# Optimization experiments

Measured on AMD Instinct MI355X. Metric: run time of the kernel, lower is better.

Reference implementation:

```python
import jax, jax.numpy as jnp
import numpy as np
from jax import lax

DIM, HEADS, HID = 192, 8, int(192 * 2.66)  # HID = 510
B, H, W = 8, 128, 128


def _ln(x, w, b):
    # WithBias LayerNorm over channel dim (to_3d puts C last, so per-pixel over C)
    mu = x.mean(1, keepdims=True)
    var = ((x - mu) ** 2).mean(1, keepdims=True)
    return (x - mu) / jnp.sqrt(var + 1e-5) * w[None, :, None, None] + b[None, :, None, None]


def _c1(x, w):  # 1x1 conv, w: [O, C]
    return jnp.einsum('bchw,oc->bohw', x, w)


def _dw(x, w):  # depthwise 3x3, w: [C, 1, 3, 3]
    return lax.conv_general_dilated(x, w, (1, 1), 'SAME',
                                    dimension_numbers=('NCHW', 'OIHW', 'NCHW'),
                                    feature_group_count=x.shape[1])


def _film(x, k_v, Wk):
    m = k_v @ Wk.T                       # [b, 2c]
    c = x.shape[1]
    return x * m[:, :c, None, None] + m[:, c:, None, None]


def _double_norm(t):
    # custom_normalize (norm + eps) followed by F.normalize (max(norm, eps)), dim=-1
    n1 = jnp.sqrt((t * t).sum(-1, keepdims=True)) + 1e-12
    t = t / n1
    n2 = jnp.sqrt((t * t).sum(-1, keepdims=True))
    return t / jnp.maximum(n2, 1e-12)


def setup_inputs() -> dict:
    key = jax.random.key(0)
    ks = jax.random.split(key, 12)
    s = 0.05
    return {
        'x': jax.random.normal(ks[0], (B, DIM, H, W), jnp.float32),
        'k_v': jax.random.normal(ks[1], (B, 256), jnp.float32),
        'ln1_w': jnp.ones((DIM,), jnp.float32),
        'ln1_b': jnp.zeros((DIM,), jnp.float32),
        'attn_kern': jax.random.normal(ks[2], (2 * DIM, 256), jnp.float32) * 0.02,
        'qkv_w': jax.random.normal(ks[3], (3 * DIM, DIM), jnp.float32) * s,
        'qkv_dw_w': jax.random.normal(ks[4], (3 * DIM, 1, 3, 3), jnp.float32) * s,
        'proj_w': jax.random.normal(ks[5], (DIM, DIM), jnp.float32) * s,
        'temperature': jnp.ones((HEADS, 1, 1), jnp.float32),
        'ln2_w': jnp.ones((DIM,), jnp.float32),
        'ln2_b': jnp.zeros((DIM,), jnp.float32),
        'ffn_kern': jax.random.normal(ks[6], (2 * DIM, 256), jnp.float32) * 0.02,
        'pin_w': jax.random.normal(ks[7], (2 * HID, DIM), jnp.float32) * s,
        'ffn_dw_w': jax.random.normal(ks[8], (2 * HID, 1, 3, 3), jnp.float32) * s,
        'pout_w': jax.random.normal(ks[9], (DIM, HID), jnp.float32) * s,
    }


def reference(x, k_v, ln1_w, ln1_b, attn_kern, qkv_w, qkv_dw_w, proj_w, temperature,
              ln2_w, ln2_b, ffn_kern, pin_w, ffn_dw_w, pout_w):
    b, c, h, w = x.shape
    cf = c // HEADS

    # ---- attention branch ----
    xn = _film(_ln(x, ln1_w, ln1_b), k_v, attn_kern)
    qkv = _dw(_c1(xn, qkv_w), qkv_dw_w)              # [b, 3c, h, w]
    q, k, v = jnp.split(qkv, 3, axis=1)
    q = _double_norm(q.reshape(b, HEADS, cf, h * w))
    k = _double_norm(k.reshape(b, HEADS, cf, h * w))
    v = v.reshape(b, HEADS, cf, h * w)
    attn = jnp.einsum('bhcn,bhdn->bhcd', q, k) * temperature  # channel attention [b,H,cf,cf]
    attn = jax.nn.softmax(attn, axis=-1)
    out = jnp.einsum('bhcd,bhdn->bhcn', attn, v).reshape(b, c, h, w)
    x = x + _c1(out, proj_w)

    # ---- gated conv FFN branch ----
    xn = _film(_ln(x, ln2_w, ln2_b), k_v, ffn_kern)
    u = _dw(_c1(xn, pin_w), ffn_dw_w)                # [b, 2*HID, h, w]
    u1, u2 = jnp.split(u, 2, axis=1)
    u = jax.nn.gelu(u1, approximate=False) * u2
    x = x + _c1(u, pout_w)
    return x  # k_v passes through unchanged
```

## Files before the change

kernel.cpp:

```cpp
#include <hip/hip_runtime.h>
#include <math.h>

#define NB 8
#define NC 192
#define NHEADS 8
#define NCF 24
#define NHW 16384
#define NWID 128
#define CQKV 576
#define OQKV_PAD 640
#define CPIN 1024
#define CG 512
#define OM_PAD 256

typedef unsigned short bfu;
typedef _Float16 f16x8 __attribute__((ext_vector_type(8)));
typedef _Float16 f16x2 __attribute__((ext_vector_type(2)));
typedef float f32x4 __attribute__((ext_vector_type(4)));

__device__ __forceinline__ unsigned short f2h(float f) {
    _Float16 h = (_Float16)f;
    return __builtin_bit_cast(unsigned short, h);
}
__device__ __forceinline__ float h2f(unsigned short u) {
    return (float)__builtin_bit_cast(_Float16, u);
}
__device__ __forceinline__ float gelu_tanh(float x) {
    float x3 = x * x * x;
    float z = 0.7978845608028654f * fmaf(0.044715f, x3, x);
    float e = __expf(2.f * z);
    float th = 1.f - 2.f / (e + 1.f);
    return 0.5f * x * (1.f + th);
}

struct F8 { float v[8]; };
union H8 { uint4 u; f16x2 h[4]; };
__device__ __forceinline__ F8 loadh8(const bfu* p) {
    uint4 r = *(const uint4*)p;
    F8 o;
    o.v[0] = h2f((unsigned short)(r.x & 0xffff)); o.v[1] = h2f((unsigned short)(r.x >> 16));
    o.v[2] = h2f((unsigned short)(r.y & 0xffff)); o.v[3] = h2f((unsigned short)(r.y >> 16));
    o.v[4] = h2f((unsigned short)(r.z & 0xffff)); o.v[5] = h2f((unsigned short)(r.z >> 16));
    o.v[6] = h2f((unsigned short)(r.w & 0xffff)); o.v[7] = h2f((unsigned short)(r.w >> 16));
    return o;
}
__device__ __forceinline__ void storeh8(bfu* p, const float* a) {
    uint4 r;
    r.x = (unsigned)f2h(a[0]) | ((unsigned)f2h(a[1]) << 16);
    r.y = (unsigned)f2h(a[2]) | ((unsigned)f2h(a[3]) << 16);
    r.z = (unsigned)f2h(a[4]) | ((unsigned)f2h(a[5]) << 16);
    r.w = (unsigned)f2h(a[6]) | ((unsigned)f2h(a[7]) << 16);
    *(uint4*)p = r;
}
__device__ __forceinline__ f16x2 h2z() {
    f16x2 z; z[0] = (_Float16)0.f; z[1] = (_Float16)0.f; return z;
}

__global__ __launch_bounds__(256) void zfill(float* __restrict__ p, int n) {
    int i = blockIdx.x * 256 + threadIdx.x;
    if (i < n) p[i] = 0.f;
}

__global__ __launch_bounds__(256) void prep_film(
    const float* __restrict__ kv, const float* __restrict__ kern,
    const float* __restrict__ lnw, const float* __restrict__ lnb,
    float* __restrict__ sArr, float* __restrict__ tArr)
{
    const int b = blockIdx.y;
    const int wave = threadIdx.x >> 6, lane = threadIdx.x & 63;
    const int r = blockIdx.x * 4 + wave;
    const float* kvb = kv + b * 256;
    float4 kvv = *(const float4*)(kvb + lane * 4);
    float4 k1 = *(const float4*)(kern + (size_t)r * 256 + lane * 4);
    float4 k2 = *(const float4*)(kern + (size_t)(r + NC) * 256 + lane * 4);
    float d1 = kvv.x * k1.x + kvv.y * k1.y + kvv.z * k1.z + kvv.w * k1.w;
    float d2 = kvv.x * k2.x + kvv.y * k2.y + kvv.z * k2.z + kvv.w * k2.w;
    #pragma unroll
    for (int off = 32; off; off >>= 1) {
        d1 += __shfl_down(d1, off, 64);
        d2 += __shfl_down(d2, off, 64);
    }
    if (lane == 0) {
        sArr[b * NC + r] = lnw[r] * d1;
        tArr[b * NC + r] = lnb[r] * d1 + d2;
    }
}

__global__ __launch_bounds__(256) void wprep(
    const float* __restrict__ W, const float* __restrict__ sA, const float* __restrict__ tA,
    bfu* __restrict__ Abf, float* __restrict__ u, float* __restrict__ v0, int mode)
{
    const int wave = threadIdx.x >> 6, lane = threadIdx.x & 63;
    const int o = blockIdx.x * 4 + wave;
    const int b = blockIdx.y;
    const int Opad = (mode == 0) ? OQKV_PAD : (mode == 1 ? CPIN : OM_PAD);
    const int K = (mode == 2) ? 512 : 192;
    const int Kr = (mode == 2) ? 510 : 192;
    const int K32 = K >> 5;
    int src;
    if (mode == 0) src = (o < 576) ? o : -1;
    else if (mode == 1) src = (o < 510) ? o : (o < 512 ? -1 : (o < 1022 ? o - 2 : -1));
    else src = (o < 192) ? o : -1;
    const float* wr = (src >= 0) ? W + (size_t)src * Kr : nullptr;
    const float* sb = sA + b * NC;
    const float* tb = tA + b * NC;
    bfu* abase = Abf + (size_t)b * Opad * K;
    float au = 0.f, av = 0.f;
    for (int c0 = lane * 4; c0 < K; c0 += 256) {
        float a[4] = {0.f, 0.f, 0.f, 0.f};
        if (src >= 0) {
            #pragma unroll
            for (int j = 0; j < 4; ++j) {
                int c = c0 + j;
                if (c < Kr) {
                    float w = wr[c];
                    if (mode == 2) a[j] = w;
                    else { a[j] = w * sb[c]; av = fmaf(w, tb[c], av); }
                }
            }
        }
        ushort4 pk;
        bfu b0 = f2h(a[0]), b1 = f2h(a[1]), b2 = f2h(a[2]), b3 = f2h(a[3]);
        pk.x = b0; pk.y = b1; pk.z = b2; pk.w = b3;
        au += h2f(b0) + h2f(b1) + h2f(b2) + h2f(b3);
        int frag = (o >> 4) * K32 + (c0 >> 5);
        int within = ((c0 >> 3) & 3) * 128 + (o & 15) * 8 + (c0 & 7);
        *(ushort4*)(abase + (size_t)frag * 512 + within) = pk;
    }
    if (mode < 2) {
        #pragma unroll
        for (int off = 32; off; off >>= 1) {
            au += __shfl_down(au, off, 64);
            av += __shfl_down(av, off, 64);
        }
        if (lane == 0) {
            u[(size_t)b * Opad + o] = au;
            v0[(size_t)b * Opad + o] = (src >= 0) ? av : 0.f;
        }
    }
}

__global__ __launch_bounds__(256) void wdw_prep(
    const float* __restrict__ src, bfu* __restrict__ dstT, int C, int mode)
{
    int i = blockIdx.x * 256 + threadIdx.x;
    if (i >= 9 * C) return;
    int tap = i / C, col = i % C;
    float v;
    if (mode == 0) v = src[(size_t)col * 9 + tap];
    else {
        if (col < 512) v = (col < 510) ? src[(size_t)col * 9 + tap] : 0.f;
        else { int c2 = col - 512; v = (c2 < 510) ? src[(size_t)(510 + c2) * 9 + tap] : 0.f; }
    }
    dstT[(size_t)tap * C + col] = f2h(v);
}

__global__ __launch_bounds__(256) void ln_cvt_cm(
    const float* __restrict__ x, float* __restrict__ mu, float* __restrict__ rstd,
    bfu* __restrict__ xbf, int cb)
{
    __shared__ bfu lt[64][198];
    const int blkpx = blockIdx.x;
    const int b = blkpx >> 8;
    const int n0 = (blkpx & 255) * 64;
    const int tid = threadIdx.x;
    #pragma unroll
    for (int it = 0; it < 12; ++it) {
        int task = it * 256 + tid;
        int c = task >> 4, q = task & 15;
        float4 v = *(const float4*)(x + ((size_t)b * NC + c) * NHW + n0 + q * 4);
        lt[q * 4 + 0][c] = f2h(v.x);
        lt[q * 4 + 1][c] = f2h(v.y);
        lt[q * 4 + 2][c] = f2h(v.z);
        lt[q * 4 + 3][c] = f2h(v.w);
    }
    __syncthreads();
    {
        int px = tid >> 2, part = tid & 3;
        const unsigned* row = (const unsigned*)&lt[px][0];
        float s = 0.f, ss = 0.f;
        #pragma unroll
        for (int i = 0; i < 24; ++i) {
            unsigned w = row[part * 24 + i];
            float a = h2f((unsigned short)(w & 0xffff));
            float bb = h2f((unsigned short)(w >> 16));
            s += a + bb; ss = fmaf(a, a, ss); ss = fmaf(bb, bb, ss);
        }
        s += __shfl_down(s, 2, 4); ss += __shfl_down(ss, 2, 4);
        s += __shfl_down(s, 1, 4); ss += __shfl_down(ss, 1, 4);
        if (part == 0) {
            int idx = b * NHW + n0 + px;
            float m = s * (1.f / 192.f);
            float var = ss * (1.f / 192.f) - m * m;
            mu[idx] = m;
            rstd[idx] = rsqrtf(var + 1e-5f);
        }
    }
    #pragma unroll
    for (int it = 0; it < 6; ++it) {
        int task = it * 256 + tid;
        int px = task / 24, ckk = task % 24;
        const unsigned* row = (const unsigned*)&lt[px][0];
        uint4 o;
        o.x = row[ckk * 4 + 0]; o.y = row[ckk * 4 + 1];
        o.z = row[ckk * 4 + 2]; o.w = row[ckk * 4 + 3];
        *(uint4*)(xbf + ((size_t)b * NHW + n0 + px) * NC + ckk * 8) = o;
    }
}

__global__ __launch_bounds__(256) void ln_stats_pm8(
    const bfu* __restrict__ xpm, float* __restrict__ mu, float* __restrict__ rstd, int cb)
{
    int gt = blockIdx.x * 256 + threadIdx.x;
    int px = gt >> 3, seg = gt & 7;
    if (px >= cb * NHW) return;
    const bfu* row = xpm + (size_t)px * NC;
    float s = 0.f, ss = 0.f;
    #pragma unroll
    for (int it = 0; it < 3; ++it) {
        F8 v = loadh8(row + (seg + it * 8) * 8);
        #pragma unroll
        for (int j = 0; j < 8; ++j) { s += v.v[j]; ss = fmaf(v.v[j], v.v[j], ss); }
    }
    #pragma unroll
    for (int off = 4; off; off >>= 1) {
        s += __shfl_down(s, off, 8);
        ss += __shfl_down(ss, off, 8);
    }
    if (seg == 0) {
        float m = s * (1.f / 192.f);
        float var = ss * (1.f / 192.f) - m * m;
        mu[px] = m;
        rstd[px] = rsqrtf(var + 1e-5f);
    }
}

template<int EPI>
__global__ __launch_bounds__(256) void gemm_pm(
    const bfu* __restrict__ A, long aBStride, int Opad, int Oreal, int K,
    const bfu* __restrict__ X, int xRow, int xOff,
    void* __restrict__ Y, int yRow,
    const void* __restrict__ res, int resRow,
    const float* __restrict__ mu, const float* __restrict__ rstd,
    const float* __restrict__ uvec, const float* __restrict__ v0vec, int uStride)
{
    constexpr bool FULLK = (EPI != 3);
    constexpr int SMEMSZ = FULLK ? (64 * 208 * 2) : 33024;
    __shared__ __align__(16) char smem[SMEMSZ];
    bfu* xs = (bfu*)smem;
    bfu (*stg)[136] = (bfu(*)[136])smem;
    float (*stg32)[129] = (float(*)[129])smem;

    const int b = blockIdx.z;
    const int om = blockIdx.y * 128;
    const int n0 = blockIdx.x * 64;
    const int tid = threadIdx.x;
    const int lane = tid & 63, wave = tid >> 6;
    const int wy = wave >> 1, wx = wave & 1;
    const int l15 = lane & 15, kg = lane >> 4;
    const int K32 = K >> 5;
    const int o16b = (om >> 4) + wy * 4;

    const bfu* Ab = A + (size_t)b * aBStride;
    const bfu* Xbase = X + ((size_t)b * NHW + n0) * xRow + xOff;

    f32x4 acc[4][2];
    #pragma unroll
    for (int i = 0; i < 4; ++i)
        #pragma unroll
        for (int j = 0; j < 2; ++j) acc[i][j] = (f32x4){0.f, 0.f, 0.f, 0.f};

    if constexpr (FULLK) {
        #pragma unroll
        for (int i = 0; i < 6; ++i) {
            int task = i * 256 + tid;
            int r = task / 24, c = task % 24;
            uint4 v = *(const uint4*)(Xbase + (size_t)r * xRow + c * 8);
            *(uint4*)&xs[r * 208 + c * 8] = v;
        }
        __syncthreads();
        #pragma unroll
        for (int k32 = 0; k32 < 6; ++k32) {
            f16x8 af[4], bfr[2];
            #pragma unroll
            for (int mf = 0; mf < 4; ++mf)
                af[mf] = *(const f16x8*)(Ab + ((size_t)(o16b + mf) * 6 + k32) * 512 + lane * 8);
            #pragma unroll
            for (int nf = 0; nf < 2; ++nf)
                bfr[nf] = *(const f16x8*)&xs[(wx * 32 + nf * 16 + l15) * 208 + k32 * 32 + kg * 8];
            #pragma unroll
            for (int mf = 0; mf < 4; ++mf)
                #pragma unroll
                for (int nf = 0; nf < 2; ++nf)
                    acc[mf][nf] = __builtin_amdgcn_mfma_f32_16x16x32_f16(af[mf], bfr[nf], acc[mf][nf], 0, 0, 0);
        }
        __syncthreads();
    } else {
        const int sr = tid >> 3, sc = tid & 7;
        const int NCH = K >> 6;
        #pragma unroll
        for (int i = 0; i < 2; ++i) {
            int r = i * 32 + sr;
            uint4 v = *(const uint4*)(Xbase + (size_t)r * xRow + sc * 8);
            *(uint4*)&xs[r * 72 + sc * 8] = v;
        }
        __syncthreads();
        for (int kc = 0; kc < NCH; ++kc) {
            const int cur = kc & 1;
            if (kc + 1 < NCH) {
                #pragma unroll
                for (int i = 0; i < 2; ++i) {
                    int r = i * 32 + sr;
                    uint4 v = *(const uint4*)(Xbase + (size_t)r * xRow + (kc + 1) * 64 + sc * 8);
                    *(uint4*)&xs[((cur ^ 1) * 64 + r) * 72 + sc * 8] = v;
                }
            }
            #pragma unroll
            for (int ks = 0; ks < 2; ++ks) {
                const int k32 = kc * 2 + ks;
                f16x8 af[4], bfr[2];
                #pragma unroll
                for (int mf = 0; mf < 4; ++mf)
                    af[mf] = *(const f16x8*)(Ab + ((size_t)(o16b + mf) * K32 + k32) * 512 + lane * 8);
                #pragma unroll
                for (int nf = 0; nf < 2; ++nf)
                    bfr[nf] = *(const f16x8*)&xs[(cur * 64 + wx * 32 + nf * 16 + l15) * 72 + ks * 32 + kg * 8];
                #pragma unroll
                for (int mf = 0; mf < 4; ++mf)
                    #pragma unroll
                    for (int nf = 0; nf < 2; ++nf)
                        acc[mf][nf] = __builtin_amdgcn_mfma_f32_16x16x32_f16(af[mf], bfr[nf], acc[mf][nf], 0, 0, 0);
            }
            __syncthreads();
        }
    }

    #pragma unroll
    for (int nf = 0; nf < 2; ++nf) {
        const int nl = wx * 32 + nf * 16 + l15;
        float muv = 0.f, rsv = 0.f;
        if (EPI == 0) {
            muv = mu[(size_t)b * NHW + n0 + nl];
            rsv = rstd[(size_t)b * NHW + n0 + nl];
        }
        #pragma unroll
        for (int mf = 0; mf < 4; ++mf) {
            const int obl = wy * 64 + mf * 16 + kg * 4;
            if (EPI == 3) {
                stg32[nl][obl + 0] = acc[mf][nf][0];
                stg32[nl][obl + 1] = acc[mf][nf][1];
                stg32[nl][obl + 2] = acc[mf][nf][2];
                stg32[nl][obl + 3] = acc[mf][nf][3];
            } else {
                float r0, r1, r2, r3;
                if (EPI == 0) {
                    float4 uv = *(const float4*)(uvec + (size_t)b * uStride + om + obl);
                    float4 vv = *(const float4*)(v0vec + (size_t)b * uStride + om + obl);
                    r0 = rsv * (acc[mf][nf][0] - muv * uv.x) + vv.x;
                    r1 = rsv * (acc[mf][nf][1] - muv * uv.y) + vv.y;
                    r2 = rsv * (acc[mf][nf][2] - muv * uv.z) + vv.z;
                    r3 = rsv * (acc[mf][nf][3] - muv * uv.w) + vv.w;
                } else {
                    r0 = acc[mf][nf][0]; r1 = acc[mf][nf][1];
                    r2 = acc[mf][nf][2]; r3 = acc[mf][nf][3];
                }
                ushort4 pk;
                pk.x = f2h(r0); pk.y = f2h(r1); pk.z = f2h(r2); pk.w = f2h(r3);
                *(ushort4*)&stg[nl][obl] = pk;
            }
        }
    }
    __syncthreads();

    if (EPI == 3) {
        #pragma unroll
        for (int it = 0; it < 8; ++it) {
            int task = it * 256 + tid;
            int o = task >> 4, q = task & 15;
            int oc = om + o;
            if (oc >= Oreal) continue;
            float vals[4];
            #pragma unroll
            for (int j = 0; j < 4; ++j) {
                float v = stg32[q * 4 + j][o];
                float r = h2f(((const bfu*)res)[((size_t)b * NHW + n0 + q * 4 + j) * resRow + oc]);
                vals[j] = v + r;
            }
            *(float4*)((float*)Y + ((size_t)b * NC + oc) * NHW + n0 + q * 4) =
                make_float4(vals[0], vals[1], vals[2], vals[3]);
        }
    } else {
        #pragma unroll
        for (int it = 0; it < 4; ++it) {
            int task = it * 256 + tid;
            int nl = task >> 4, ch = task & 15;
            int oc = om + ch * 8;
            if (oc >= Oreal) continue;
            uint4 sv = *(const uint4*)&stg[nl][ch * 8];
            size_t nglob = (size_t)b * NHW + n0 + nl;
            if (EPI == 0) {
                *(uint4*)((bfu*)Y + nglob * yRow + oc) = sv;
            } else {
                float a[8];
                a[0] = h2f((unsigned short)(sv.x & 0xffff)); a[1] = h2f((unsigned short)(sv.x >> 16));
                a[2] = h2f((unsigned short)(sv.y & 0xffff)); a[3] = h2f((unsigned short)(sv.y >> 16));
                a[4] = h2f((unsigned short)(sv.z & 0xffff)); a[5] = h2f((unsigned short)(sv.z >> 16));
                a[6] = h2f((unsigned short)(sv.w & 0xffff)); a[7] = h2f((unsigned short)(sv.w >> 16));
                F8 rv = loadh8((const bfu*)res + nglob * resRow + oc);
                #pragma unroll
                for (int j = 0; j < 8; ++j) a[j] += rv.v[j];
                storeh8((bfu*)Y + nglob * yRow + oc, a);
            }
        }
    }
}

template<int CIN>
__global__ __launch_bounds__(256) void dw_pm8(
    const bfu* __restrict__ in, const bfu* __restrict__ wT, bfu* __restrict__ out, int cb)
{
    const int CHUNKS = CIN / 8;
    const int NPB = NHW / 8;
    int f = blockIdx.x * 256 + threadIdx.x;
    if (f >= cb * NPB * CHUNKS) return;
    int ch = f % CHUNKS;
    int pb = f / CHUNKS;
    int n8 = pb & (NPB - 1);
    int b  = pb >> 11;
    int xq = n8 & 15, y = n8 >> 4;
    int x0 = xq * 8;
    const int c8 = ch * 8;
    const bfu* rowb = in + ((size_t)b * NHW + (size_t)y * NWID) * CIN + c8;

    f16x2 acc[8][4];
    #pragma unroll
    for (int j = 0; j < 8; ++j)
        #pragma unroll
        for (int q = 0; q < 4; ++q) acc[j][q] = h2z();

    #pragma unroll
    for (int dy = -1; dy <= 1; ++dy) {
        int yy = y + dy;
        if ((unsigned)yy >= (unsigned)NWID) continue;
        const bfu* rb = rowb + (long)dy * NWID * CIN;
        f16x2 w1[3][4];
        #pragma unroll
        for (int t = 0; t < 3; ++t) {
            H8 wv; wv.u = *(const uint4*)(wT + (size_t)((dy + 1) * 3 + t) * CIN + c8);
            #pragma unroll
            for (int q = 0; q < 4; ++q) w1[t][q] = wv.h[q];
        }
        #pragma unroll
        for (int c = 0; c < 10; ++c) {
            int xx = x0 - 1 + c;
            if ((unsigned)xx >= (unsigned)NWID) continue;
            H8 v; v.u = *(const uint4*)(rb + (size_t)xx * CIN);
            #pragma unroll
            for (int j = 0; j < 8; ++j) {
                int t = c - j;
                if (t < 0 || t > 2) continue;
                #pragma unroll
                for (int q = 0; q < 4; ++q)
                    acc[j][q] = w1[t][q] * v.h[q] + acc[j][q];
            }
        }
    }
    #pragma unroll
    for (int j = 0; j < 8; ++j) {
        H8 o;
        #pragma unroll
        for (int q = 0; q < 4; ++q) o.h[q] = acc[j][q];
        *(uint4*)(out + ((size_t)b * NHW + (size_t)y * NWID + x0 + j) * CIN + c8) = o.u;
    }
}

template<int CIN, int COUT>
__global__ __launch_bounds__(256) void dw_gate(
    const bfu* __restrict__ in, const bfu* __restrict__ wT, bfu* __restrict__ out, int cb)
{
    const int CHUNKS = COUT / 8;
    const int NPB = NHW / 4;
    int f = blockIdx.x * 256 + threadIdx.x;
    if (f >= cb * NPB * CHUNKS) return;
    int ch = f % CHUNKS;
    int pb = f / CHUNKS;
    int n4 = pb & (NPB - 1);
    int b  = pb >> 12;
    int xb = n4 & 31, y = n4 >> 5;
    int x0 = xb * 4;
    const int c8 = ch * 8;
    const bfu* rowb = in + ((size_t)b * NHW + (size_t)y * NWID) * CIN + c8;

    f16x2 a1[4][4], a2[4][4];
    #pragma unroll
    for (int j = 0; j < 4; ++j)
        #pragma unroll
        for (int q = 0; q < 4; ++q) { a1[j][q] = h2z(); a2[j][q] = h2z(); }

    #pragma unroll
    for (int dy = -1; dy <= 1; ++dy) {
        int yy = y + dy;
        if ((unsigned)yy >= (unsigned)NWID) continue;
        const bfu* rb = rowb + (long)dy * NWID * CIN;
        f16x2 w1[3][4], w2[3][4];
        #pragma unroll
        for (int t = 0; t < 3; ++t) {
            const bfu* wp = wT + (size_t)((dy + 1) * 3 + t) * CIN + c8;
            H8 wa; wa.u = *(const uint4*)wp;
            H8 wb; wb.u = *(const uint4*)(wp + 512);
            #pragma unroll
            for (int q = 0; q < 4; ++q) { w1[t][q] = wa.h[q]; w2[t][q] = wb.h[q]; }
        }
        #pragma unroll
        for (int c = 0; c < 6; ++c) {
            int xx = x0 - 1 + c;
            if ((unsigned)xx >= (unsigned)NWID) continue;
            H8 v1; v1.u = *(const uint4*)(rb + (size_t)xx * CIN);
            H8 v2; v2.u = *(const uint4*)(rb + (size_t)xx * CIN + 512);
            #pragma unroll
            for (int j = 0; j < 4; ++j) {
                int t = c - j;
                if (t < 0 || t > 2) continue;
                #pragma unroll
                for (int q = 0; q < 4; ++q) {
                    a1[j][q] = w1[t][q] * v1.h[q] + a1[j][q];
                    a2[j][q] = w2[t][q] * v2.h[q] + a2[j][q];
                }
            }
        }
    }
    #pragma unroll
    for (int j = 0; j < 4; ++j) {
        H8 o;
        #pragma unroll
        for (int q = 0; q < 4; ++q) {
            float g0 = gelu_tanh((float)a1[j][q][0]) * (float)a2[j][q][0];
            float g1 = gelu_tanh((float)a1[j][q][1]) * (float)a2[j][q][1];
            f16x2 r; r[0] = (_Float16)g0; r[1] = (_Float16)g1;
            o.h[q] = r;
        }
        *(uint4*)(out + ((size_t)b * NHW + (size_t)y * NWID + x0 + j) * COUT + c8) = o.u;
    }
}

__global__ __launch_bounds__(256) void gram_pm(
    const bfu* __restrict__ qkv, float* __restrict__ S32,
    float* __restrict__ Q2, float* __restrict__ K2, int b0)
{
    __shared__ bfu lds[392 * 72];
    const int b = blockIdx.y;
    const int nc = blockIdx.x;
    const int tid = threadIdx.x;
    const int lane = tid & 63, wave = tid >> 6;
    const int l15 = lane & 15, kg = lane >> 4;

    f32x4 sAcc[2][2][2], qAcc[2][2], kAcc[2][2];
    #pragma unroll
    for (int h = 0; h < 2; ++h)
        #pragma unroll
        for (int i = 0; i < 2; ++i) {
            qAcc[h][i] = (f32x4){0.f, 0.f, 0.f, 0.f};
            kAcc[h][i] = (f32x4){0.f, 0.f, 0.f, 0.f};
            #pragma unroll
            for (int j = 0; j < 2; ++j) sAcc[h][i][j] = (f32x4){0.f, 0.f, 0.f, 0.f};
        }

    const size_t pbase = (size_t)b * NHW + (size_t)nc * 256;
    unsigned* ldsw = (unsigned*)lds;

    for (int it = 0; it < 4; ++it) {
        const size_t nb = pbase + it * 64;
        #pragma unroll
        for (int i = 0; i < 6; ++i) {
            int task = i * 256 + tid;
            int np = task & 31, ch = task >> 5;
            const bfu* r0 = qkv + (nb + np * 2) * CQKV + ch * 8;
            uint4 v0 = *(const uint4*)r0;
            uint4 v1 = *(const uint4*)(r0 + CQKV);
            int cb8 = ch * 8;
            ldsw[(cb8 + 0) * 36 + np] = (v0.x & 0xffffu) | (v1.x << 16);
            ldsw[(cb8 + 1) * 36 + np] = (v0.x >> 16) | (v1.x & 0xffff0000u);
            ldsw[(cb8 + 2) * 36 + np] = (v0.y & 0xffffu) | (v1.y << 16);
            ldsw[(cb8 + 3) * 36 + np] = (v0.y >> 16) | (v1.y & 0xffff0000u);
            ldsw[(cb8 + 4) * 36 + np] = (v0.z & 0xffffu) | (v1.z << 16);
            ldsw[(cb8 + 5) * 36 + np] = (v0.z >> 16) | (v1.z & 0xffff0000u);
            ldsw[(cb8 + 6) * 36 + np] = (v0.w & 0xffffu) | (v1.w << 16);
            ldsw[(cb8 + 7) * 36 + np] = (v0.w >> 16) | (v1.w & 0xffff0000u);
        }
        ldsw[(384 + (tid >> 5)) * 36 + (tid & 31)] = 0;
        __syncthreads();
        #pragma unroll
        for (int hh = 0; hh < 2; ++hh) {
            const int h = wave * 2 + hh;
            const int qr = h * NCF, kr = NC + h * NCF;
            #pragma unroll
            for (int ks = 0; ks < 2; ++ks) {
                const int nsub = ks * 32 + kg * 8;
                f16x8 aq0 = *(const f16x8*)(lds + (qr + l15) * 72 + nsub);
                f16x8 aq1 = *(const f16x8*)(lds + (qr + 16 + l15) * 72 + nsub);
                f16x8 bk0 = *(const f16x8*)(lds + (kr + l15) * 72 + nsub);
                f16x8 bk1 = *(const f16x8*)(lds + (kr + 16 + l15) * 72 + nsub);
                sAcc[hh][0][0] = __builtin_amdgcn_mfma_f32_16x16x32_f16(aq0, bk0, sAcc[hh][0][0], 0, 0, 0);
                sAcc[hh][0][1] = __builtin_amdgcn_mfma_f32_16x16x32_f16(aq0, bk1, sAcc[hh][0][1], 0, 0, 0);
                sAcc[hh][1][0] = __builtin_amdgcn_mfma_f32_16x16x32_f16(aq1, bk0, sAcc[hh][1][0], 0, 0, 0);
                sAcc[hh][1][1] = __builtin_amdgcn_mfma_f32_16x16x32_f16(aq1, bk1, sAcc[hh][1][1], 0, 0, 0);
                qAcc[hh][0] = __builtin_amdgcn_mfma_f32_16x16x32_f16(aq0, aq0, qAcc[hh][0], 0, 0, 0);
                qAcc[hh][1] = __builtin_amdgcn_mfma_f32_16x16x32_f16(aq1, aq1, qAcc[hh][1], 0, 0, 0);
                kAcc[hh][0] = __builtin_amdgcn_mfma_f32_16x16x32_f16(bk0, bk0, kAcc[hh][0], 0, 0, 0);
                kAcc[hh][1] = __builtin_amdgcn_mfma_f32_16x16x32_f16(bk1, bk1, kAcc[hh][1], 0, 0, 0);
            }
        }
        __syncthreads();
    }

    const int gb = b0 + b;
    #pragma unroll
    for (int hh = 0; hh < 2; ++hh) {
        const int h = wave * 2 + hh;
        float* Sp = S32 + ((size_t)gb * NHEADS + h) * 1024;
        #pragma unroll
        for (int mt = 0; mt < 2; ++mt)
            #pragma unroll
            for (int nt = 0; nt < 2; ++nt)
                #pragma unroll
                for (int r = 0; r < 4; ++r) {
                    int c = mt * 16 + kg * 4 + r, d = nt * 16 + l15;
                    atomicAdd(&Sp[c * 32 + d], sAcc[hh][mt][nt][r]);
                }
        #pragma unroll
        for (int t = 0; t < 2; ++t)
            #pragma unroll
            for (int r = 0; r < 4; ++r) {
                int row = t * 16 + kg * 4 + r, col = t * 16 + l15;
                if (row == col && row < NCF) {
                    atomicAdd(&Q2[((size_t)gb * NHEADS + h) * NCF + row], qAcc[hh][t][r]);
                    atomicAdd(&K2[((size_t)gb * NHEADS + h) * NCF + row], kAcc[hh][t][r]);
                }
            }
    }
}

__global__ __launch_bounds__(256) void attn_fold(
    const float* __restrict__ S32, const float* __restrict__ Q2, const float* __restrict__ K2,
    const float* __restrict__ temp, const float* __restrict__ projw, bfu* __restrict__ Mbf, int b0)
{
    const int gb = b0 + blockIdx.x, tid = threadIdx.x;
    __shared__ float P[NHEADS * NCF * NCF];
    for (int e = tid; e < NHEADS * NCF * NCF; e += 256) {
        int h = e / (NCF * NCF);
        int r = e % (NCF * NCF);
        int c = r / NCF, d = r % NCF;
        float sv = S32[((size_t)gb * NHEADS + h) * 1024 + c * 32 + d];
        float rq = sqrtf(Q2[((size_t)gb * NHEADS + h) * NCF + c]);
        float rk = sqrtf(K2[((size_t)gb * NHEADS + h) * NCF + d]);
        P[e] = sv / (rq * rk) * temp[h];
    }
    __syncthreads();
    if (tid < NHEADS * NCF) {
        int h = tid / NCF, c = tid % NCF;
        float* row = P + h * (NCF * NCF) + c * NCF;
        float mx = row[0];
        #pragma unroll
        for (int d = 1; d < NCF; ++d) mx = fmaxf(mx, row[d]);
        float sum = 0.f;
        #pragma unroll
        for (int d = 0; d < NCF; ++d) { float e2 = __expf(row[d] - mx); row[d] = e2; sum += e2; }
        float inv = 1.f / sum;
        #pragma unroll
        for (int d = 0; d < NCF; ++d) row[d] *= inv;
    }
    __syncthreads();
    bfu* Mb = Mbf + (size_t)gb * OM_PAD * NC;
    if (tid < NC) {
        int o = tid;
        int o16 = o >> 4, l15o = o & 15;
        for (int h = 0; h < NHEADS; ++h) {
            float pw[NCF];
            #pragma unroll
            for (int c = 0; c < NCF; ++c) pw[c] = projw[(size_t)o * NC + h * NCF + c];
            #pragma unroll
            for (int d = 0; d < NCF; ++d) {
                float acc = 0.f;
                #pragma unroll
                for (int c = 0; c < NCF; ++c) acc = fmaf(pw[c], P[h * (NCF * NCF) + c * NCF + d], acc);
                int cc = h * NCF + d;
                int idx = (o16 * 6 + (cc >> 5)) * 512 + ((cc >> 3) & 3) * 128 + l15o * 8 + (cc & 7);
                Mb[idx] = f2h(acc);
            }
        }
    }
    for (int e = tid; e < (OM_PAD - NC) * NC; e += 256) Mb[NC * NC + e] = 0;
}

extern "C" void kernel_launch(void* const* d_in, const int* in_sizes, int n_in,
                              void* d_out, int out_size, void* d_ws, size_t ws_size,
                              hipStream_t stream)
{
    const float* x     = (const float*)d_in[0];
    const float* kv    = (const float*)d_in[1];
    const float* ln1w  = (const float*)d_in[2];
    const float* ln1b  = (const float*)d_in[3];
    const float* akern = (const float*)d_in[4];
    const float* qkvw  = (const float*)d_in[5];
    const float* qkvdw = (const float*)d_in[6];
    const float* projw = (const float*)d_in[7];
    const float* temp  = (const float*)d_in[8];
    const float* ln2w  = (const float*)d_in[9];
    const float* ln2b  = (const float*)d_in[10];
    const float* fkern = (const float*)d_in[11];
    const float* pinw  = (const float*)d_in[12];
    const float* ffndw = (const float*)d_in[13];
    const float* poutw = (const float*)d_in[14];
    float* out = (float*)d_out;

    char* wp = (char*)d_ws;
    size_t off = 0;
    auto take = [&](size_t bytes) {
        char* r = wp + off;
        off = (off + bytes + 255) & ~(size_t)255;
        return r;
    };
    float* mu1   = (float*)take((size_t)NB * NHW * 4);
    float* rstd1 = (float*)take((size_t)NB * NHW * 4);
    float* mu2   = (float*)take((size_t)NB * NHW * 4);
    float* rstd2 = (float*)take((size_t)NB * NHW * 4);
    float* s1 = (float*)take(NB * NC * 4);  float* t1 = (float*)take(NB * NC * 4);
    float* s2 = (float*)take(NB * NC * 4);  float* t2 = (float*)take(NB * NC * 4);
    bfu* A1 = (bfu*)take((size_t)NB * OQKV_PAD * 192 * 2);
    bfu* A2 = (bfu*)take((size_t)NB * CPIN * 192 * 2);
    bfu* A3 = (bfu*)take((size_t)OM_PAD * 512 * 2);
    bfu* Mbf = (bfu*)take((size_t)NB * OM_PAD * NC * 2);
    float* u1  = (float*)take((size_t)NB * OQKV_PAD * 4);
    float* v01 = (float*)take((size_t)NB * OQKV_PAD * 4);
    float* u2  = (float*)take((size_t)NB * CPIN * 4);
    float* v02 = (float*)take((size_t)NB * CPIN * 4);
    bfu* wdwT1 = (bfu*)take(9 * CQKV * 2);
    bfu* wdwT2 = (bfu*)take(9 * CPIN * 2);
    float* S32 = (float*)take((size_t)NB * NHEADS * 1024 * 4);
    float* Q2  = (float*)take((size_t)NB * NHEADS * NCF * 4);
    float* K2  = (float*)take((size_t)NB * NHEADS * NCF * 4);
    const size_t bigoff = off;

    const size_t PB = (size_t)NHW * (384 + 384 + 2048 + 1152);
    size_t avail = (ws_size > bigoff) ? ws_size - bigoff : 0;
    int CB = 8;
    while (CB > 1 && (size_t)CB * PB > avail) CB >>= 1;

    dim3 blk(256);

    prep_film<<<dim3(48, NB), blk, 0, stream>>>(kv, akern, ln1w, ln1b, s1, t1);
    prep_film<<<dim3(48, NB), blk, 0, stream>>>(kv, fkern, ln2w, ln2b, s2, t2);
    wprep<<<dim3(OQKV_PAD / 4, NB), blk, 0, stream>>>(qkvw, s1, t1, A1, u1, v01, 0);
    wprep<<<dim3(CPIN / 4, NB), blk, 0, stream>>>(pinw, s2, t2, A2, u2, v02, 1);
    wprep<<<dim3(OM_PAD / 4, 1), blk, 0, stream>>>(poutw, s1, t1, A3, nullptr, nullptr, 2);
    wdw_prep<<<(9 * CQKV + 255) / 256, blk, 0, stream>>>(qkvdw, wdwT1, CQKV, 0);
    wdw_prep<<<(9 * CPIN + 255) / 256, blk, 0, stream>>>(ffndw, wdwT2, CPIN, 1);
    {
        int nz = NB * NHEADS * 1024 + 2 * NB * NHEADS * NCF + 256;
        zfill<<<(nz + 255) / 256, blk, 0, stream>>>(S32, nz);
    }

    for (int b0 = 0; b0 < NB; b0 += CB) {
        bfu* bfX  = (bfu*)(wp + bigoff);
        bfu* out1 = (bfu*)(wp + bigoff + (size_t)CB * NHW * 384);
        char* big1 = wp + bigoff + (size_t)CB * NHW * 768;
        char* big2 = big1 + (size_t)CB * NHW * 2048;
        bfu* qkv_pre = (bfu*)big1;
        bfu* qkvb    = (bfu*)big2;
        bfu* u_pre   = (bfu*)big1;
        bfu* gbuf    = (bfu*)big2;

        const float* xb = x + (size_t)b0 * NC * NHW;
        float* mu1b = mu1 + (size_t)b0 * NHW;   float* rs1b = rstd1 + (size_t)b0 * NHW;
        float* mu2b = mu2 + (size_t)b0 * NHW;   float* rs2b = rstd2 + (size_t)b0 * NHW;

        ln_cvt_cm<<<CB * 256, blk, 0, stream>>>(xb, mu1b, rs1b, bfX, CB);
        gemm_pm<0><<<dim3(256, OQKV_PAD / 128, CB), blk, 0, stream>>>(
            A1 + (size_t)b0 * OQKV_PAD * 192, (long)OQKV_PAD * 192, OQKV_PAD, CQKV, 192,
            bfX, NC, 0, qkv_pre, CQKV, nullptr, 0,
            mu1b, rs1b, u1 + (size_t)b0 * OQKV_PAD, v01 + (size_t)b0 * OQKV_PAD, OQKV_PAD);
        dw_pm8<CQKV><<<CB * 576, blk, 0, stream>>>(qkv_pre, wdwT1, qkvb, CB);
        gram_pm<<<dim3(64, CB), blk, 0, stream>>>(qkvb, S32, Q2, K2, b0);
        attn_fold<<<CB, blk, 0, stream>>>(S32, Q2, K2, temp, projw, Mbf, b0);
        gemm_pm<1><<<dim3(256, OM_PAD / 128, CB), blk, 0, stream>>>(
            Mbf + (size_t)b0 * OM_PAD * NC, (long)OM_PAD * NC, OM_PAD, NC, 192,
            qkvb, CQKV, 384, out1, NC, bfX, NC,
            nullptr, nullptr, nullptr, nullptr, 0);

        ln_stats_pm8<<<CB * 512, blk, 0, stream>>>(out1, mu2b, rs2b, CB);
        gemm_pm<0><<<dim3(256, CPIN / 128, CB), blk, 0, stream>>>(
            A2 + (size_t)b0 * CPIN * 192, (long)CPIN * 192, CPIN, CPIN, 192,
            out1, NC, 0, u_pre, CPIN, nullptr, 0,
            mu2b, rs2b, u2 + (size_t)b0 * CPIN, v02 + (size_t)b0 * CPIN, CPIN);
        dw_gate<CPIN, CG><<<CB * (NHW / 4) * (CG / 8) / 256, blk, 0, stream>>>(
            u_pre, wdwT2, gbuf, CB);
        gemm_pm<3><<<dim3(256, OM_PAD / 128, CB), blk, 0, stream>>>(
            A3, 0, OM_PAD, NC, 512,
            gbuf, CG, 0, out + (size_t)b0 * NC * NHW, 0, out1, NC,
            nullptr, nullptr, nullptr, nullptr, 0);
    }
}
```

Before: 800.9 us.

## Fuse LayerNorm stats into GEMM, widen GEMM N-tile, and widen dw_gate pixel strip

LayerNorm mean/rstd computation moves out of ln_cvt_cm and the separate ln_stats_pm8 kernel and into the full-K GEMM. The GEMM now computes the statistics from its shared-memory X tile. The full-K GEMM tile grows from 64 to 128 pixels per block, doubling accumulators per wave and halving the grid. The depthwise gate kernel now processes 8 pixels per thread instead of 4, so each loaded input column is reused across more outputs. These changes remove a kernel launch and the global mu/rstd round-trips, at the cost of higher register use and more shared memory per block, which may lower occupancy.

```diff
diff --git a/kernel.cpp b/kernel.cpp
--- a/kernel.cpp
+++ b/kernel.cpp
@@ -156,8 +156,7 @@
 }
 
 __global__ __launch_bounds__(256) void ln_cvt_cm(
-    const float* __restrict__ x, float* __restrict__ mu, float* __restrict__ rstd,
-    bfu* __restrict__ xbf, int cb)
+    const float* __restrict__ x, bfu* __restrict__ xbf, int cb)
 {
     __shared__ bfu lt[64][198];
     const int blkpx = blockIdx.x;
@@ -175,27 +174,6 @@
         lt[q * 4 + 3][c] = f2h(v.w);
     }
     __syncthreads();
-    {
-        int px = tid >> 2, part = tid & 3;
-        const unsigned* row = (const unsigned*)&lt[px][0];
-        float s = 0.f, ss = 0.f;
-        #pragma unroll
-        for (int i = 0; i < 24; ++i) {
-            unsigned w = row[part * 24 + i];
-            float a = h2f((unsigned short)(w & 0xffff));
-            float bb = h2f((unsigned short)(w >> 16));
-            s += a + bb; ss = fmaf(a, a, ss); ss = fmaf(bb, bb, ss);
-        }
-        s += __shfl_down(s, 2, 4); ss += __shfl_down(ss, 2, 4);
-        s += __shfl_down(s, 1, 4); ss += __shfl_down(ss, 1, 4);
-        if (part == 0) {
-            int idx = b * NHW + n0 + px;
-            float m = s * (1.f / 192.f);
-            float var = ss * (1.f / 192.f) - m * m;
-            mu[idx] = m;
-            rstd[idx] = rsqrtf(var + 1e-5f);
-        }
-    }
     #pragma unroll
     for (int it = 0; it < 6; ++it) {
         int task = it * 256 + tid;
@@ -208,150 +186,96 @@
     }
 }
 
-__global__ __launch_bounds__(256) void ln_stats_pm8(
-    const bfu* __restrict__ xpm, float* __restrict__ mu, float* __restrict__ rstd, int cb)
-{
-    int gt = blockIdx.x * 256 + threadIdx.x;
-    int px = gt >> 3, seg = gt & 7;
-    if (px >= cb * NHW) return;
-    const bfu* row = xpm + (size_t)px * NC;
-    float s = 0.f, ss = 0.f;
-    #pragma unroll
-    for (int it = 0; it < 3; ++it) {
-        F8 v = loadh8(row + (seg + it * 8) * 8);
-        #pragma unroll
-        for (int j = 0; j < 8; ++j) { s += v.v[j]; ss = fmaf(v.v[j], v.v[j], ss); }
-    }
-    #pragma unroll
-    for (int off = 4; off; off >>= 1) {
-        s += __shfl_down(s, off, 8);
-        ss += __shfl_down(ss, off, 8);
-    }
-    if (seg == 0) {
-        float m = s * (1.f / 192.f);
-        float var = ss * (1.f / 192.f) - m * m;
-        mu[px] = m;
-        rstd[px] = rsqrtf(var + 1e-5f);
-    }
-}
-
 template<int EPI>
 __global__ __launch_bounds__(256) void gemm_pm(
     const bfu* __restrict__ A, long aBStride, int Opad, int Oreal, int K,
     const bfu* __restrict__ X, int xRow, int xOff,
     void* __restrict__ Y, int yRow,
     const void* __restrict__ res, int resRow,
-    const float* __restrict__ mu, const float* __restrict__ rstd,
     const float* __restrict__ uvec, const float* __restrict__ v0vec, int uStride)
 {
     constexpr bool FULLK = (EPI != 3);
-    constexpr int SMEMSZ = FULLK ? (64 * 208 * 2) : 33024;
+    constexpr int SMEMSZ = FULLK ? (128 * 200 * 2 + 128 * 8) : 33024;
     __shared__ __align__(16) char smem[SMEMSZ];
     bfu* xs = (bfu*)smem;
     bfu (*stg)[136] = (bfu(*)[136])smem;
     float (*stg32)[129] = (float(*)[129])smem;
+    float* smu = (float*)(smem + 128 * 200 * 2);
+    float* srs = smu + 128;
 
     const int b = blockIdx.z;
     const int om = blockIdx.y * 128;
-    const int n0 = blockIdx.x * 64;
     const int tid = threadIdx.x;
     const int lane = tid & 63, wave = tid >> 6;
     const int wy = wave >> 1, wx = wave & 1;
     const int l15 = lane & 15, kg = lane >> 4;
     const int K32 = K >> 5;
     const int o16b = (om >> 4) + wy * 4;
-
     const bfu* Ab = A + (size_t)b * aBStride;
-    const bfu* Xbase = X + ((size_t)b * NHW + n0) * xRow + xOff;
-
-    f32x4 acc[4][2];
-    #pragma unroll
-    for (int i = 0; i < 4; ++i)
-        #pragma unroll
-        for (int j = 0; j < 2; ++j) acc[i][j] = (f32x4){0.f, 0.f, 0.f, 0.f};
 
     if constexpr (FULLK) {
-        #pragma unroll
-        for (int i = 0; i < 6; ++i) {
+        const int n0 = blockIdx.x * 128;
+        const bfu* Xbase = X + ((size_t)b * NHW + n0) * xRow + xOff;
+
+        f32x4 acc[4][4];
+        #pragma unroll
+        for (int i = 0; i < 4; ++i)
+            #pragma unroll
+            for (int j = 0; j < 4; ++j) acc[i][j] = (f32x4){0.f, 0.f, 0.f, 0.f};
+
+        #pragma unroll
+        for (int i = 0; i < 12; ++i) {
             int task = i * 256 + tid;
             int r = task / 24, c = task % 24;
             uint4 v = *(const uint4*)(Xbase + (size_t)r * xRow + c * 8);
-            *(uint4*)&xs[r * 208 + c * 8] = v;
+            *(uint4*)&xs[r * 200 + c * 8] = v;
         }
         __syncthreads();
+
+        if (EPI == 0) {
+            int px = tid >> 1, hh = tid & 1;
+            float s = 0.f, ss = 0.f;
+            #pragma unroll
+            for (int i = 0; i < 12; ++i) {
+                F8 v = loadh8(xs + px * 200 + hh * 96 + i * 8);
+                #pragma unroll
+                for (int j = 0; j < 8; ++j) { s += v.v[j]; ss = fmaf(v.v[j], v.v[j], ss); }
+            }
+            s += __shfl_xor(s, 1, 64);
+            ss += __shfl_xor(ss, 1, 64);
+            if (hh == 0) {
+                float m = s * (1.f / 192.f);
+                float var = ss * (1.f / 192.f) - m * m;
+                smu[px] = m;
+                srs[px] = rsqrtf(var + 1e-5f);
+            }
+        }
+
         #pragma unroll
         for (int k32 = 0; k32 < 6; ++k32) {
-            f16x8 af[4], bfr[2];
+            f16x8 af[4], bfr[4];
             #pragma unroll
             for (int mf = 0; mf < 4; ++mf)
                 af[mf] = *(const f16x8*)(Ab + ((size_t)(o16b + mf) * 6 + k32) * 512 + lane * 8);
             #pragma unroll
-            for (int nf = 0; nf < 2; ++nf)
-                bfr[nf] = *(const f16x8*)&xs[(wx * 32 + nf * 16 + l15) * 208 + k32 * 32 + kg * 8];
+            for (int nf = 0; nf < 4; ++nf)
+                bfr[nf] = *(const f16x8*)&xs[(wx * 64 + nf * 16 + l15) * 200 + k32 * 32 + kg * 8];
             #pragma unroll
             for (int mf = 0; mf < 4; ++mf)
                 #pragma unroll
-                for (int nf = 0; nf < 2; ++nf)
+                for (int nf = 0; nf < 4; ++nf)
                     acc[mf][nf] = __builtin_amdgcn_mfma_f32_16x16x32_f16(af[mf], bfr[nf], acc[mf][nf], 0, 0, 0);
         }
         __syncthreads();
-    } else {
-        const int sr = tid >> 3, sc = tid & 7;
-        const int NCH = K >> 6;
-        #pragma unroll
-        for (int i = 0; i < 2; ++i) {
-            int r = i * 32 + sr;
-            uint4 v = *(const uint4*)(Xbase + (size_t)r * xRow + sc * 8);
-            *(uint4*)&xs[r * 72 + sc * 8] = v;
-        }
-        __syncthreads();
-        for (int kc = 0; kc < NCH; ++kc) {
-            const int cur = kc & 1;
-            if (kc + 1 < NCH) {
-                #pragma unroll
-                for (int i = 0; i < 2; ++i) {
-                    int r = i * 32 + sr;
-                    uint4 v = *(const uint4*)(Xbase + (size_t)r * xRow + (kc + 1) * 64 + sc * 8);
-                    *(uint4*)&xs[((cur ^ 1) * 64 + r) * 72 + sc * 8] = v;
-                }
-            }
-            #pragma unroll
-            for (int ks = 0; ks < 2; ++ks) {
-                const int k32 = kc * 2 + ks;
-                f16x8 af[4], bfr[2];
-                #pragma unroll
-                for (int mf = 0; mf < 4; ++mf)
-                    af[mf] = *(const f16x8*)(Ab + ((size_t)(o16b + mf) * K32 + k32) * 512 + lane * 8);
-                #pragma unroll
-                for (int nf = 0; nf < 2; ++nf)
-                    bfr[nf] = *(const f16x8*)&xs[(cur * 64 + wx * 32 + nf * 16 + l15) * 72 + ks * 32 + kg * 8];
-                #pragma unroll
-                for (int mf = 0; mf < 4; ++mf)
-                    #pragma unroll
-                    for (int nf = 0; nf < 2; ++nf)
-                        acc[mf][nf] = __builtin_amdgcn_mfma_f32_16x16x32_f16(af[mf], bfr[nf], acc[mf][nf], 0, 0, 0);
-            }
-            __syncthreads();
-        }
-    }
-
-    #pragma unroll
-    for (int nf = 0; nf < 2; ++nf) {
-        const int nl = wx * 32 + nf * 16 + l15;
-        float muv = 0.f, rsv = 0.f;
-        if (EPI == 0) {
-            muv = mu[(size_t)b * NHW + n0 + nl];
-            rsv = rstd[(size_t)b * NHW + n0 + nl];
-        }
-        #pragma unroll
-        for (int mf = 0; mf < 4; ++mf) {
-            const int obl = wy * 64 + mf * 16 + kg * 4;
-            if (EPI == 3) {
-                stg32[nl][obl + 0] = acc[mf][nf][0];
-                stg32[nl][obl + 1] = acc[mf][nf][1];
-                stg32[nl][obl + 2] = acc[mf][nf][2];
-                stg32[nl][obl + 3] = acc[mf][nf][3];
-            } else {
+
+        #pragma unroll
+        for (int nf = 0; nf < 4; ++nf) {
+            const int nl = wx * 64 + nf * 16 + l15;
+            float muv = 0.f, rsv = 0.f;
+            if (EPI == 0) { muv = smu[nl]; rsv = srs[nl]; }
+            #pragma unroll
+            for (int mf = 0; mf < 4; ++mf) {
+                const int obl = wy * 64 + mf * 16 + kg * 4;
                 float r0, r1, r2, r3;
                 if (EPI == 0) {
                     float4 uv = *(const float4*)(uvec + (size_t)b * uStride + om + obl);
@@ -369,29 +293,10 @@
                 *(ushort4*)&stg[nl][obl] = pk;
             }
         }
-    }
-    __syncthreads();
-
-    if (EPI == 3) {
+        __syncthreads();
+
         #pragma unroll
         for (int it = 0; it < 8; ++it) {
-            int task = it * 256 + tid;
-            int o = task >> 4, q = task & 15;
-            int oc = om + o;
-            if (oc >= Oreal) continue;
-            float vals[4];
-            #pragma unroll
-            for (int j = 0; j < 4; ++j) {
-                float v = stg32[q * 4 + j][o];
-                float r = h2f(((const bfu*)res)[((size_t)b * NHW + n0 + q * 4 + j) * resRow + oc]);
-                vals[j] = v + r;
-            }
-            *(float4*)((float*)Y + ((size_t)b * NC + oc) * NHW + n0 + q * 4) =
-                make_float4(vals[0], vals[1], vals[2], vals[3]);
-        }
-    } else {
-        #pragma unroll
-        for (int it = 0; it < 4; ++it) {
             int task = it * 256 + tid;
             int nl = task >> 4, ch = task & 15;
             int oc = om + ch * 8;
@@ -412,6 +317,84 @@
                 storeh8((bfu*)Y + nglob * yRow + oc, a);
             }
         }
+    } else {
+        const int n0 = blockIdx.x * 64;
+        const bfu* Xbase = X + ((size_t)b * NHW + n0) * xRow + xOff;
+        const int sr = tid >> 3, sc = tid & 7;
+        const int NCH = K >> 6;
+
+        f32x4 acc[4][2];
+        #pragma unroll
+        for (int i = 0; i < 4; ++i)
+            #pragma unroll
+            for (int j = 0; j < 2; ++j) acc[i][j] = (f32x4){0.f, 0.f, 0.f, 0.f};
+
+        #pragma unroll
+        for (int i = 0; i < 2; ++i) {
+            int r = i * 32 + sr;
+            uint4 v = *(const uint4*)(Xbase + (size_t)r * xRow + sc * 8);
+            *(uint4*)&xs[r * 72 + sc * 8] = v;
+        }
+        __syncthreads();
+        for (int kc = 0; kc < NCH; ++kc) {
+            const int cur = kc & 1;
+            if (kc + 1 < NCH) {
+                #pragma unroll
+                for (int i = 0; i < 2; ++i) {
+                    int r = i * 32 + sr;
+                    uint4 v = *(const uint4*)(Xbase + (size_t)r * xRow + (kc + 1) * 64 + sc * 8);
+                    *(uint4*)&xs[((cur ^ 1) * 64 + r) * 72 + sc * 8] = v;
+                }
+            }
+            #pragma unroll
+            for (int ks = 0; ks < 2; ++ks) {
+                const int k32 = kc * 2 + ks;
+                f16x8 af[4], bfr[2];
+                #pragma unroll
+                for (int mf = 0; mf < 4; ++mf)
+                    af[mf] = *(const f16x8*)(Ab + ((size_t)(o16b + mf) * K32 + k32) * 512 + lane * 8);
+                #pragma unroll
+                for (int nf = 0; nf < 2; ++nf)
+                    bfr[nf] = *(const f16x8*)&xs[(cur * 64 + wx * 32 + nf * 16 + l15) * 72 + ks * 32 + kg * 8];
+                #pragma unroll
+                for (int mf = 0; mf < 4; ++mf)
+                    #pragma unroll
+                    for (int nf = 0; nf < 2; ++nf)
+                        acc[mf][nf] = __builtin_amdgcn_mfma_f32_16x16x32_f16(af[mf], bfr[nf], acc[mf][nf], 0, 0, 0);
+            }
+            __syncthreads();
+        }
+
+        #pragma unroll
+        for (int nf = 0; nf < 2; ++nf) {
+            const int nl = wx * 32 + nf * 16 + l15;
+            #pragma unroll
+            for (int mf = 0; mf < 4; ++mf) {
+                const int obl = wy * 64 + mf * 16 + kg * 4;
+                stg32[nl][obl + 0] = acc[mf][nf][0];
+                stg32[nl][obl + 1] = acc[mf][nf][1];
+                stg32[nl][obl + 2] = acc[mf][nf][2];
+                stg32[nl][obl + 3] = acc[mf][nf][3];
+            }
+        }
+        __syncthreads();
+
+        #pragma unroll
+        for (int it = 0; it < 8; ++it) {
+            int task = it * 256 + tid;
+            int o = task >> 4, q = task & 15;
+            int oc = om + o;
+            if (oc >= Oreal) continue;
+            float vals[4];
+            #pragma unroll
+            for (int j = 0; j < 4; ++j) {
+                float v = stg32[q * 4 + j][o];
+                float r = h2f(((const bfu*)res)[((size_t)b * NHW + n0 + q * 4 + j) * resRow + oc]);
+                vals[j] = v + r;
+            }
+            *(float4*)((float*)Y + ((size_t)b * NC + oc) * NHW + n0 + q * 4) =
+                make_float4(vals[0], vals[1], vals[2], vals[3]);
+        }
     }
 }
 
@@ -475,25 +458,25 @@
 }
 
 template<int CIN, int COUT>
-__global__ __launch_bounds__(256) void dw_gate(
+__global__ __launch_bounds__(256) void dw_gate8(
     const bfu* __restrict__ in, const bfu* __restrict__ wT, bfu* __restrict__ out, int cb)
 {
     const int CHUNKS = COUT / 8;
-    const int NPB = NHW / 4;
+    const int NPB = NHW / 8;
     int f = blockIdx.x * 256 + threadIdx.x;
     if (f >= cb * NPB * CHUNKS) return;
     int ch = f % CHUNKS;
     int pb = f / CHUNKS;
-    int n4 = pb & (NPB - 1);
-    int b  = pb >> 12;
-    int xb = n4 & 31, y = n4 >> 5;
-    int x0 = xb * 4;
+    int n8 = pb & (NPB - 1);
+    int b  = pb >> 11;
+    int xq = n8 & 15, y = n8 >> 4;
+    int x0 = xq * 8;
     const int c8 = ch * 8;
     const bfu* rowb = in + ((size_t)b * NHW + (size_t)y * NWID) * CIN + c8;
 
-    f16x2 a1[4][4], a2[4][4];
-    #pragma unroll
-    for (int j = 0; j < 4; ++j)
+    f16x2 a1[8][4], a2[8][4];
+    #pragma unroll
+    for (int j = 0; j < 8; ++j)
         #pragma unroll
         for (int q = 0; q < 4; ++q) { a1[j][q] = h2z(); a2[j][q] = h2z(); }
 
@@ -512,13 +495,13 @@
             for (int q = 0; q < 4; ++q) { w1[t][q] = wa.h[q]; w2[t][q] = wb.h[q]; }
         }
         #pragma unroll
-        for (int c = 0; c < 6; ++c) {
+        for (int c = 0; c < 10; ++c) {
             int xx = x0 - 1 + c;
             if ((unsigned)xx >= (unsigned)NWID) continue;
             H8 v1; v1.u = *(const uint4*)(rb + (size_t)xx * CIN);
             H8 v2; v2.u = *(const uint4*)(rb + (size_t)xx * CIN + 512);
             #pragma unroll
-            for (int j = 0; j < 4; ++j) {
+            for (int j = 0; j < 8; ++j) {
                 int t = c - j;
                 if (t < 0 || t > 2) continue;
                 #pragma unroll
@@ -530,7 +513,7 @@
         }
     }
     #pragma unroll
-    for (int j = 0; j < 4; ++j) {
+    for (int j = 0; j < 8; ++j) {
         H8 o;
         #pragma unroll
         for (int q = 0; q < 4; ++q) {
@@ -720,10 +703,6 @@
         off = (off + bytes + 255) & ~(size_t)255;
         return r;
     };
-    float* mu1   = (float*)take((size_t)NB * NHW * 4);
-    float* rstd1 = (float*)take((size_t)NB * NHW * 4);
-    float* mu2   = (float*)take((size_t)NB * NHW * 4);
-    float* rstd2 = (float*)take((size_t)NB * NHW * 4);
     float* s1 = (float*)take(NB * NC * 4);  float* t1 = (float*)take(NB * NC * 4);
     float* s2 = (float*)take(NB * NC * 4);  float* t2 = (float*)take(NB * NC * 4);
     bfu* A1 = (bfu*)take((size_t)NB * OQKV_PAD * 192 * 2);
@@ -771,32 +750,28 @@
         bfu* gbuf    = (bfu*)big2;
 
         const float* xb = x + (size_t)b0 * NC * NHW;
-        float* mu1b = mu1 + (size_t)b0 * NHW;   float* rs1b = rstd1 + (size_t)b0 * NHW;
-        float* mu2b = mu2 + (size_t)b0 * NHW;   float* rs2b = rstd2 + (size_t)b0 * NHW;
-
-        ln_cvt_cm<<<CB * 256, blk, 0, stream>>>(xb, mu1b, rs1b, bfX, CB);
-        gemm_pm<0><<<dim3(256, OQKV_PAD / 128, CB), blk, 0, stream>>>(
+
+        ln_cvt_cm<<<CB * 256, blk, 0, stream>>>(xb, bfX, CB);
+        gemm_pm<0><<<dim3(128, OQKV_PAD / 128, CB), blk, 0, stream>>>(
             A1 + (size_t)b0 * OQKV_PAD * 192, (long)OQKV_PAD * 192, OQKV_PAD, CQKV, 192,
             bfX, NC, 0, qkv_pre, CQKV, nullptr, 0,
-            mu1b, rs1b, u1 + (size_t)b0 * OQKV_PAD, v01 + (size_t)b0 * OQKV_PAD, OQKV_PAD);
+            u1 + (size_t)b0 * OQKV_PAD, v01 + (size_t)b0 * OQKV_PAD, OQKV_PAD);
         dw_pm8<CQKV><<<CB * 576, blk, 0, stream>>>(qkv_pre, wdwT1, qkvb, CB);
         gram_pm<<<dim3(64, CB), blk, 0, stream>>>(qkvb, S32, Q2, K2, b0);
         attn_fold<<<CB, blk, 0, stream>>>(S32, Q2, K2, temp, projw, Mbf, b0);
-        gemm_pm<1><<<dim3(256, OM_PAD / 128, CB), blk, 0, stream>>>(
+        gemm_pm<1><<<dim3(128, OM_PAD / 128, CB), blk, 0, stream>>>(
             Mbf + (size_t)b0 * OM_PAD * NC, (long)OM_PAD * NC, OM_PAD, NC, 192,
             qkvb, CQKV, 384, out1, NC, bfX, NC,
-            nullptr, nullptr, nullptr, nullptr, 0);
-
-        ln_stats_pm8<<<CB * 512, blk, 0, stream>>>(out1, mu2b, rs2b, CB);
-        gemm_pm<0><<<dim3(256, CPIN / 128, CB), blk, 0, stream>>>(
+            nullptr, nullptr, 0);
+
+        gemm_pm<0><<<dim3(128, CPIN / 128, CB), blk, 0, stream>>>(
             A2 + (size_t)b0 * CPIN * 192, (long)CPIN * 192, CPIN, CPIN, 192,
             out1, NC, 0, u_pre, CPIN, nullptr, 0,
-            mu2b, rs2b, u2 + (size_t)b0 * CPIN, v02 + (size_t)b0 * CPIN, CPIN);
-        dw_gate<CPIN, CG><<<CB * (NHW / 4) * (CG / 8) / 256, blk, 0, stream>>>(
-            u_pre, wdwT2, gbuf, CB);
+            u2 + (size_t)b0 * CPIN, v02 + (size_t)b0 * CPIN, CPIN);
+        dw_gate8<CPIN, CG><<<CB * 512, blk, 0, stream>>>(u_pre, wdwT2, gbuf, CB);
         gemm_pm<3><<<dim3(256, OM_PAD / 128, CB), blk, 0, stream>>>(
             A3, 0, OM_PAD, NC, 512,
             gbuf, CG, 0, out + (size_t)b0 * NC * NHW, 0, out1, NC,
-            nullptr, nullptr, nullptr, nullptr, 0);
-    }
-}
+            nullptr, nullptr, 0);
+    }
+}
```

Result: no change. 785.3 us (-2.0%).
